# Kernel tuning notes

Hardware: AMD Instinct MI355X
Metric: run time of the kernel (lower is better)

## Reference

```python
import jax, jax.numpy as jnp
import numpy as np

EMBED = 1024
HEADS = 16
NQ = 32        # n_qubits_transformer
NQF = 32       # n_qubits_ffn
DK = NQ // HEADS
EPS = 1e-5


def layernorm(x, g, b):
    mu = jnp.mean(x, axis=-1, keepdims=True)
    var = jnp.var(x, axis=-1, keepdims=True)
    return (x - mu) * jax.lax.rsqrt(var + EPS) * g + b


def setup_inputs() -> dict:
    key = jax.random.key(0)
    ks = jax.random.split(key, 6)
    B, S = 8, 1024
    return {
        "x": jax.random.normal(ks[0], (B, S, EMBED), dtype=jnp.float32),
        "theta_attn": jax.random.normal(ks[1], (NQ,), dtype=jnp.float32),
        "theta_ffn": jax.random.normal(ks[2], (NQF,), dtype=jnp.float32),
        "w_combine": jax.random.normal(ks[3], (EMBED, NQ), dtype=jnp.float32) * 0.05,
        "w_ffn1": jax.random.normal(ks[4], (4096, NQF), dtype=jnp.float32) * 0.05,
        "w_ffn2": jax.random.normal(ks[5], (EMBED, 4096), dtype=jnp.float32) * 0.02,
        "g1": jnp.ones((EMBED,), jnp.float32),
        "b1": jnp.zeros((EMBED,), jnp.float32),
        "g2": jnp.ones((EMBED,), jnp.float32),
        "b2": jnp.zeros((EMBED,), jnp.float32),
    }


def quantum_measure(x_slice, theta):
    # |0> -RX(x)-> -RY(theta)-> <Z>  ==  cos(theta) * cos(x)  per wire (no entanglement)
    return jnp.cos(theta) * jnp.cos(x_slice)


def reference(x, theta_attn, theta_ffn, w_combine, w_ffn1, w_ffn2, g1, b1, g2, b2):
    B, S, _ = x.shape
    # --- quantum multi-head attention (q = k = v from circuit measurements) ---
    qv = quantum_measure(x[..., :NQ], theta_attn)                    # [B,S,NQ]
    q = qv.reshape(B, S, HEADS, DK).transpose(0, 2, 1, 3)            # [B,H,S,dk]
    scores = jnp.einsum("bhsd,bhtd->bhst", q, q) / jnp.sqrt(jnp.float32(DK))
    probs = jax.nn.softmax(scores, axis=-1)
    attn = jnp.einsum("bhst,bhtd->bhsd", probs, q)                   # [B,H,S,dk]
    attn = attn.transpose(0, 2, 1, 3).reshape(B, S, NQ)
    attn = attn @ w_combine.T                                        # [B,S,E]
    x1 = layernorm(x + attn, g1, b1)
    # --- quantum feed-forward ---
    qf = quantum_measure(x1[..., :NQF], theta_ffn)                   # [B,S,NQF]
    h = jax.nn.relu(qf @ w_ffn1.T)                                   # [B,S,ffn]
    ffn = h @ w_ffn2.T                                               # [B,S,E]
    return layernorm(x1 + ffn, g2, b2)
```

## Files before the change

kernel.cpp:

```cpp
#include <hip/hip_runtime.h>
#include <math.h>

#define EMB   1024
#define S_LEN 1024
#define NQ    32
#define HEADS 16
#define FFN   4096
#define T_TOK 8192
#define EPS   1e-5f
#define MiB   (1024ull * 1024ull)

typedef unsigned short u16;
typedef __attribute__((ext_vector_type(8))) short short8;
typedef __attribute__((ext_vector_type(4))) float float4_t;

__device__ __forceinline__ u16 f2bf(float f) {
    unsigned u = __float_as_uint(f);
    u += 0x7FFF + ((u >> 16) & 1);
    return (u16)(u >> 16);
}
__device__ __forceinline__ void async16(u16* lds, const u16* g) {
    __builtin_amdgcn_global_load_lds(
        (const __attribute__((address_space(1))) unsigned int*)g,
        (__attribute__((address_space(3))) unsigned int*)lds, 16, 0, 0);
}

#define N_W1 (FFN * NQ)
#define N_W2 (EMB * FFN)
#define N_WC (EMB * NQ)
__global__ __launch_bounds__(256) void k_prep(
        const float* __restrict__ w1, const float* __restrict__ w2,
        const float* __restrict__ wc, const float* __restrict__ x,
        const float* __restrict__ tha,
        u16* __restrict__ w1b, u16* __restrict__ w2b, u16* __restrict__ wcb,
        float* __restrict__ qv) {
    int idx = blockIdx.x * 256 + threadIdx.x;
    if (idx < T_TOK * NQ) {
        int i = idx & 31;
        int t = idx >> 5;
        int b = t >> 10, s = t & 1023;
        float cv = __cosf(tha[i]) * __cosf(x[(size_t)t * EMB + i]);
        int h = i >> 1, c = i & 1;
        qv[(((size_t)(b * HEADS + h)) * S_LEN + s) * 2 + c] = cv;
    }
    if (idx < N_W1)               w1b[idx] = f2bf(w1[idx]);
    else if (idx < N_W1 + N_W2)   w2b[idx - N_W1] = f2bf(w2[idx - N_W1]);
    else if (idx < N_W1 + N_W2 + N_WC) wcb[idx - N_W1 - N_W2] = f2bf(wc[idx - N_W1 - N_W2]);
}

__global__ __launch_bounds__(256) void k_attn(const float* __restrict__ qv,
                                              u16* __restrict__ attnB) {
    __shared__ __align__(16) float2 kv[S_LEN];
    int bh  = blockIdx.x;
    int tid = threadIdx.x;
    const float2* base = (const float2*)(qv + (size_t)bh * S_LEN * 2);
    for (int i = tid; i < S_LEN; i += 256) kv[i] = base[i];
    __syncthreads();
    int s = blockIdx.y * 256 + tid;
    float2 q = kv[s];
    float qx = q.x * 0.70710678f, qy = q.y * 0.70710678f;
    float den = 0.f, nx = 0.f, ny = 0.f;
#pragma unroll 4
    for (int t = 0; t < S_LEN; ++t) {
        float2 k = kv[t];
        float d = fmaf(qy, k.y, qx * k.x);
        float e = __expf(d);
        den += e;
        nx = fmaf(e, k.x, nx);
        ny = fmaf(e, k.y, ny);
    }
    float inv = 1.f / den;
    int b = bh >> 4, h = bh & 15;
    u16* o = attnB + (size_t)(b * S_LEN + s) * NQ + 2 * h;
    o[0] = f2bf(nx * inv);
    o[1] = f2bf(ny * inv);
}

__global__ __launch_bounds__(256) void k_combine_ln(
        const u16* __restrict__ A,
        const u16* __restrict__ B,
        const float* __restrict__ X,
        const float* __restrict__ g1, const float* __restrict__ b1,
        const float* __restrict__ thf,
        float* __restrict__ x1,
        u16* __restrict__ qf) {
    __shared__ float red[4][16][2];
    int tid = threadIdx.x, lane = tid & 63, wave = tid >> 6;
    int t0 = blockIdx.x * 16;
    int colbase = wave * 256;
    int rrow = (lane >> 4) * 4;
    short8 afr = *(const short8*)(A + (size_t)(t0 + (lane & 15)) * 32 + (lane >> 4) * 8);
    float4_t acc[16];
    float4_t zero = {0.f, 0.f, 0.f, 0.f};
#pragma unroll
    for (int tn = 0; tn < 16; ++tn) {
        short8 bfr = *(const short8*)(B + (size_t)(colbase + tn * 16 + (lane & 15)) * 32 + (lane >> 4) * 8);
        acc[tn] = __builtin_amdgcn_mfma_f32_16x16x32_bf16(afr, bfr, zero, 0, 0, 0);
    }
    float sm[4] = {0.f, 0.f, 0.f, 0.f}, sq[4] = {0.f, 0.f, 0.f, 0.f};
#pragma unroll
    for (int tn = 0; tn < 16; ++tn) {
        int nc = colbase + tn * 16 + (lane & 15);
#pragma unroll
        for (int r = 0; r < 4; ++r) {
            float v = acc[tn][r] + X[(size_t)(t0 + rrow + r) * EMB + nc];
            acc[tn][r] = v;
            sm[r] += v;
            sq[r] = fmaf(v, v, sq[r]);
        }
    }
#pragma unroll
    for (int o = 1; o < 16; o <<= 1) {
#pragma unroll
        for (int r = 0; r < 4; ++r) {
            sm[r] += __shfl_xor(sm[r], o, 64);
            sq[r] += __shfl_xor(sq[r], o, 64);
        }
    }
    if ((lane & 15) == 0) {
#pragma unroll
        for (int r = 0; r < 4; ++r) {
            red[wave][rrow + r][0] = sm[r];
            red[wave][rrow + r][1] = sq[r];
        }
    }
    __syncthreads();
    float mu[4], rs[4];
#pragma unroll
    for (int r = 0; r < 4; ++r) {
        float s = red[0][rrow + r][0] + red[1][rrow + r][0] +
                  red[2][rrow + r][0] + red[3][rrow + r][0];
        float q = red[0][rrow + r][1] + red[1][rrow + r][1] +
                  red[2][rrow + r][1] + red[3][rrow + r][1];
        float m = s * (1.f / EMB);
        mu[r] = m;
        rs[r] = rsqrtf(q * (1.f / EMB) - m * m + EPS);
    }
#pragma unroll
    for (int tn = 0; tn < 16; ++tn) {
        int nc = colbase + tn * 16 + (lane & 15);
        float g = g1[nc], bb = b1[nc];
#pragma unroll
        for (int r = 0; r < 4; ++r) {
            float y = (acc[tn][r] - mu[r]) * rs[r] * g + bb;
            x1[(size_t)(t0 + rrow + r) * EMB + nc] = y;
            if (nc < NQ)
                qf[(size_t)(t0 + rrow + r) * NQ + nc] = f2bf(__cosf(thf[nc]) * __cosf(y));
        }
    }
}

__global__ __launch_bounds__(256) void k_h(
        const u16* __restrict__ QF,
        const u16* __restrict__ W1,
        u16* __restrict__ H) {
    __shared__ __align__(16) u16 sA[128 * 32];
    __shared__ __align__(16) u16 sB[128 * 32];
    int tid = threadIdx.x, lane = tid & 63, wave = tid >> 6;
    int m0 = blockIdx.y * 128, n0 = blockIdx.x * 128;
    int wm = (wave >> 1) * 64, wn = (wave & 1) * 64;
    int srow = lane >> 2, scol = (lane & 3) * 8;
#pragma unroll
    for (int i = 0; i < 2; ++i) {
        int rb = wave * 32 + i * 16;
        async16(&sA[(size_t)rb * 32], QF + (size_t)(m0 + rb + srow) * 32 + scol);
        async16(&sB[(size_t)rb * 32], W1 + (size_t)(n0 + rb + srow) * 32 + scol);
    }
    __syncthreads();
    short8 af[4], bfr[4];
#pragma unroll
    for (int tm = 0; tm < 4; ++tm)
        af[tm] = *(const short8*)&sA[(size_t)(wm + tm * 16 + (lane & 15)) * 32 + (lane >> 4) * 8];
#pragma unroll
    for (int tn = 0; tn < 4; ++tn)
        bfr[tn] = *(const short8*)&sB[(size_t)(wn + tn * 16 + (lane & 15)) * 32 + (lane >> 4) * 8];
    float4_t zero = {0.f, 0.f, 0.f, 0.f};
#pragma unroll
    for (int tm = 0; tm < 4; ++tm) {
        int mr = m0 + wm + tm * 16 + (lane >> 4) * 4;
#pragma unroll
        for (int tn = 0; tn < 4; ++tn) {
            float4_t acc = __builtin_amdgcn_mfma_f32_16x16x32_bf16(af[tm], bfr[tn], zero, 0, 0, 0);
            int nc = n0 + wn + tn * 16 + (lane & 15);
#pragma unroll
            for (int r = 0; r < 4; ++r)
                H[(size_t)(mr + r) * FFN + nc] = f2bf(fmaxf(acc[r], 0.f));
        }
    }
}

__global__ __launch_bounds__(256, 2) void k_ffn2_db(
        const u16* __restrict__ H,
        const u16* __restrict__ W2,
        const float* __restrict__ X1,
        float* __restrict__ Y) {
    __shared__ __align__(16) u16 smem[32768];
    const int tid = threadIdx.x, lane = tid & 63, wave = tid >> 6;
    const int wm = wave >> 1, wn = wave & 1;

    int bid = blockIdx.x;
    int lid = (bid & 7) * 64 + (bid >> 3);
    const int m0 = (lid >> 3) * 128, n0 = (lid & 7) * 128;

    u16* A0 = smem;          u16* B0 = smem + 8192;
    u16* A1 = smem + 16384;  u16* B1 = smem + 24576;

    const int srow = tid >> 3;
    const int scol = ((tid & 7) ^ (srow & 7)) << 3;
    const int cb0 = ((0  + ((lane >> 4) * 16)) ^ ((lane & 7) << 4)) >> 1;
    const int cb1 = ((64 + ((lane >> 4) * 16)) ^ ((lane & 7) << 4)) >> 1;
    const int arow = lane & 15;

    auto stage = [&](u16* sA, u16* sB, int kt) {
#pragma unroll
        for (int j = 0; j < 4; ++j)
            async16(sA + (j * 32 + wave * 8) * 64,
                    H + (size_t)(m0 + j * 32 + srow) * FFN + kt + scol);
#pragma unroll
        for (int j = 0; j < 4; ++j)
            async16(sB + (j * 32 + wave * 8) * 64,
                    W2 + (size_t)(n0 + j * 32 + srow) * FFN + kt + scol);
    };

    float4_t acc[4][4];
    float4_t zero = {0.f, 0.f, 0.f, 0.f};
#pragma unroll
    for (int i = 0; i < 4; ++i)
#pragma unroll
        for (int j = 0; j < 4; ++j) acc[i][j] = zero;

    u16 *cA = A0, *cB = B0, *nA = A1, *nB = B1;
    stage(cA, cB, 0);

#pragma unroll 1
    for (int t = 0; t < 64; ++t) {
        if (t + 1 < 64) {
            stage(nA, nB, (t + 1) * 64);
            asm volatile("s_waitcnt vmcnt(8)" ::: "memory");
        } else {
            asm volatile("s_waitcnt vmcnt(0)" ::: "memory");
        }
        __builtin_amdgcn_s_barrier();

        short8 af0[4], af1[4], bf0[4], bf1[4];
#pragma unroll
        for (int f = 0; f < 4; ++f) {
            af0[f] = *(const short8*)(cA + (wm * 64 + f * 16 + arow) * 64 + cb0);
            af1[f] = *(const short8*)(cA + (wm * 64 + f * 16 + arow) * 64 + cb1);
        }
#pragma unroll
        for (int f = 0; f < 4; ++f) {
            bf0[f] = *(const short8*)(cB + (wn * 64 + f * 16 + arow) * 64 + cb0);
            bf1[f] = *(const short8*)(cB + (wn * 64 + f * 16 + arow) * 64 + cb1);
        }
        __builtin_amdgcn_s_setprio(1);
#pragma unroll
        for (int i = 0; i < 4; ++i)
#pragma unroll
            for (int j = 0; j < 4; ++j)
                acc[i][j] = __builtin_amdgcn_mfma_f32_16x16x32_bf16(af0[i], bf0[j], acc[i][j], 0, 0, 0);
#pragma unroll
        for (int i = 0; i < 4; ++i)
#pragma unroll
            for (int j = 0; j < 4; ++j)
                acc[i][j] = __builtin_amdgcn_mfma_f32_16x16x32_bf16(af1[i], bf1[j], acc[i][j], 0, 0, 0);
        __builtin_amdgcn_s_setprio(0);
        __builtin_amdgcn_s_barrier();

        u16* tA = cA; cA = nA; nA = tA;
        u16* tB = cB; cB = nB; nB = tB;
    }

#pragma unroll
    for (int i = 0; i < 4; ++i) {
        int mr = m0 + wm * 64 + i * 16 + (lane >> 4) * 4;
#pragma unroll
        for (int j = 0; j < 4; ++j) {
            int nc = n0 + wn * 64 + j * 16 + (lane & 15);
#pragma unroll
            for (int r = 0; r < 4; ++r) {
                size_t off = (size_t)(mr + r) * EMB + nc;
                Y[off] = acc[i][j][r] + X1[off];
            }
        }
    }
}

__global__ __launch_bounds__(256) void k_ffn_fused(
        const u16* __restrict__ QF,
        const u16* __restrict__ W1,
        const u16* __restrict__ W2,
        const float* __restrict__ X1,
        float* __restrict__ Y) {
    const int K = FFN, N = EMB;
    __shared__ __align__(16) u16 sW[64 * 32];
    __shared__ __align__(16) u16 sA[128 * 64];
    __shared__ __align__(16) u16 sB[128 * 64];
    int tid = threadIdx.x, lane = tid & 63, wave = tid >> 6;
    int m0 = blockIdx.y * 128, n0 = blockIdx.x * 128;
    int wm = (wave >> 1) * 64, wn = (wave & 1) * 64;

    short8 aq[2];
#pragma unroll
    for (int tm2 = 0; tm2 < 2; ++tm2) {
        int m = m0 + wave * 32 + tm2 * 16 + (lane & 15);
        aq[tm2] = *(const short8*)(QF + (size_t)m * 32 + (lane >> 4) * 8);
    }
    const u16* gB = W2 + (size_t)(n0 + wave * 32 + (lane >> 3)) * K + (lane & 7) * 8;
    const u16* gW = W1 + (size_t)(wave * 16 + (lane >> 2)) * 32 + (lane & 3) * 8;

    float4_t acc[4][4];
    float4_t zero = {0.f, 0.f, 0.f, 0.f};
#pragma unroll
    for (int tm = 0; tm < 4; ++tm)
#pragma unroll
        for (int tn = 0; tn < 4; ++tn) acc[tm][tn] = zero;

    for (int kt = 0; kt < K; kt += 64) {
        async16(&sW[(size_t)(wave * 16) * 32], gW + (size_t)kt * 32);
#pragma unroll
        for (int i = 0; i < 4; ++i)
            async16(&sB[(size_t)(wave * 32 + i * 8) * 64], gB + (size_t)i * 8 * K + kt);
        __syncthreads();

        int r0 = (lane >> 4) * 4;
#pragma unroll
        for (int tm2 = 0; tm2 < 2; ++tm2) {
            int mrow = wave * 32 + tm2 * 16;
#pragma unroll
            for (int tf = 0; tf < 4; ++tf) {
                short8 bw = *(const short8*)&sW[(size_t)(tf * 16 + (lane & 15)) * 32 + (lane >> 4) * 8];
                float4_t d = __builtin_amdgcn_mfma_f32_16x16x32_bf16(aq[tm2], bw, zero, 0, 0, 0);
                int cc = tf * 16 + (lane & 15);
#pragma unroll
                for (int r = 0; r < 4; ++r)
                    sA[(size_t)(mrow + r0 + r) * 64 + cc] = f2bf(fmaxf(d[r], 0.f));
            }
        }
        __syncthreads();

#pragma unroll
        for (int kk = 0; kk < 2; ++kk) {
            short8 af[4], bfr[4];
#pragma unroll
            for (int tm = 0; tm < 4; ++tm)
                af[tm] = *(const short8*)&sA[(size_t)(wm + tm * 16 + (lane & 15)) * 64 + kk * 32 + (lane >> 4) * 8];
#pragma unroll
            for (int tn = 0; tn < 4; ++tn)
                bfr[tn] = *(const short8*)&sB[(size_t)(wn + tn * 16 + (lane & 15)) * 64 + kk * 32 + (lane >> 4) * 8];
#pragma unroll
            for (int tm = 0; tm < 4; ++tm)
#pragma unroll
                for (int tn = 0; tn < 4; ++tn)
                    acc[tm][tn] = __builtin_amdgcn_mfma_f32_16x16x32_bf16(af[tm], bfr[tn], acc[tm][tn], 0, 0, 0);
        }
        __syncthreads();
    }
#pragma unroll
    for (int tm = 0; tm < 4; ++tm) {
        int mr = m0 + wm + tm * 16 + (lane >> 4) * 4;
#pragma unroll
        for (int tn = 0; tn < 4; ++tn) {
            int nc = n0 + wn + tn * 16 + (lane & 15);
#pragma unroll
            for (int r = 0; r < 4; ++r) {
                size_t off = (size_t)(mr + r) * N + nc;
                Y[off] = acc[tm][tn][r] + X1[off];
            }
        }
    }
}

__global__ __launch_bounds__(256) void k_ln2(float* __restrict__ y,
                                             const float* __restrict__ g2,
                                             const float* __restrict__ b2) {
    __shared__ float red[8];
    int t = blockIdx.x;
    int tid = threadIdx.x, lane = tid & 63, wave = tid >> 6;
    int e0 = tid * 4;
    float* row = y + (size_t)t * EMB;
    float4 v4 = *(const float4*)(row + e0);
    float v[4] = {v4.x, v4.y, v4.z, v4.w};
    float sm = v[0] + v[1] + v[2] + v[3];
    float sq = v[0]*v[0] + v[1]*v[1] + v[2]*v[2] + v[3]*v[3];
    for (int o = 32; o > 0; o >>= 1) {
        sm += __shfl_xor(sm, o, 64);
        sq += __shfl_xor(sq, o, 64);
    }
    if (lane == 0) { red[wave * 2] = sm; red[wave * 2 + 1] = sq; }
    __syncthreads();
    sm = red[0] + red[2] + red[4] + red[6];
    sq = red[1] + red[3] + red[5] + red[7];
    float mu  = sm * (1.f / EMB);
    float var = sq * (1.f / EMB) - mu * mu;
    float rs  = rsqrtf(var + EPS);
    float4 o4;
    o4.x = (v[0] - mu) * rs * g2[e0 + 0] + b2[e0 + 0];
    o4.y = (v[1] - mu) * rs * g2[e0 + 1] + b2[e0 + 1];
    o4.z = (v[2] - mu) * rs * g2[e0 + 2] + b2[e0 + 2];
    o4.w = (v[3] - mu) * rs * g2[e0 + 3] + b2[e0 + 3];
    *(float4*)(row + e0) = o4;
}

extern "C" void kernel_launch(void* const* d_in, const int* in_sizes, int n_in,
                              void* d_out, int out_size, void* d_ws, size_t ws_size,
                              hipStream_t stream) {
    const float* x   = (const float*)d_in[0];
    const float* tha = (const float*)d_in[1];
    const float* thf = (const float*)d_in[2];
    const float* wc  = (const float*)d_in[3];
    const float* w1  = (const float*)d_in[4];
    const float* w2  = (const float*)d_in[5];
    const float* g1  = (const float*)d_in[6];
    const float* b1  = (const float*)d_in[7];
    const float* g2  = (const float*)d_in[8];
    const float* b2  = (const float*)d_in[9];
    float* out = (float*)d_out;

    char* ws = (char*)d_ws;
    float* x1    = (float*)(ws);
    float* qv    = (float*)(ws + 32 * MiB);
    u16*   attnB = (u16*)  (ws + 33 * MiB);
    u16*   qf    = (u16*)  (ws + 34 * MiB);
    u16*   w1b   = (u16*)  (ws + 35 * MiB);
    u16*   w2b   = (u16*)  (ws + 36 * MiB);
    u16*   wcb   = (u16*)  (ws + 44 * MiB);
    u16*   hbuf  = (u16*)  (ws + 48 * MiB);

    const bool split = ws_size >= (size_t)112 * MiB;

    k_prep<<<(N_W1 + N_W2 + N_WC + 255) / 256, 256, 0, stream>>>(
        w1, w2, wc, x, tha, w1b, w2b, wcb, qv);
    k_attn<<<dim3(128, 4), 256, 0, stream>>>(qv, attnB);
    k_combine_ln<<<T_TOK / 16, 256, 0, stream>>>(
        attnB, wcb, x, g1, b1, thf, x1, qf);
    if (split) {
        k_h<<<dim3(FFN / 128, T_TOK / 128), 256, 0, stream>>>(qf, w1b, hbuf);
        k_ffn2_db<<<dim3(512), 256, 0, stream>>>(hbuf, w2b, x1, out);
    } else {
        k_ffn_fused<<<dim3(EMB / 128, T_TOK / 128), 256, 0, stream>>>(
            qf, w1b, w2b, x1, out);
    }
    k_ln2<<<T_TOK, 256, 0, stream>>>(out, g2, b2);
}
```

Before: 251.3 us.

## Fuse all stages into one cooperative persistent kernel with grid syncs

Replaces the sequence of six kernel launches with a single cooperative kernel of 512 blocks that runs each stage (prep, attention, combine+LN, FFN1, FFN2, LN2) separated by grid-wide syncs. The aim is to remove launch overhead and inter-kernel gaps. In exchange, stages that previously used more blocks (prep, k_h, LN2) now loop over work with a fixed grid, grid.sync adds its own cost, and occupancy is capped by the largest stage's shared memory and registers. The old multi-kernel path is kept as a fallback if the cooperative launch fails.

```diff
diff --git a/kernel.cpp b/kernel.cpp
--- a/kernel.cpp
+++ b/kernel.cpp
@@ -1,5 +1,8 @@
 #include <hip/hip_runtime.h>
+#include <hip/hip_cooperative_groups.h>
 #include <math.h>
+
+namespace cg = cooperative_groups;
 
 #define EMB   1024
 #define S_LEN 1024
@@ -28,6 +31,298 @@
 #define N_W1 (FFN * NQ)
 #define N_W2 (EMB * FFN)
 #define N_WC (EMB * NQ)
+#define NPREP ((N_W1 + N_W2 + N_WC) / 256)
+
+__global__ __launch_bounds__(256, 2) void k_mega(
+        const float* __restrict__ w1, const float* __restrict__ w2,
+        const float* __restrict__ wc, const float* __restrict__ x,
+        const float* __restrict__ tha, const float* __restrict__ thf,
+        const float* __restrict__ g1, const float* __restrict__ b1,
+        const float* __restrict__ g2, const float* __restrict__ b2,
+        u16* __restrict__ w1b, u16* __restrict__ w2b, u16* __restrict__ wcb,
+        float* __restrict__ qv, u16* __restrict__ attnB, u16* __restrict__ qf,
+        float* __restrict__ x1, u16* __restrict__ hbuf,
+        float* __restrict__ out) {
+    __shared__ __align__(16) u16 smem[32768];
+    cg::grid_group grid = cg::this_grid();
+    const int bid = blockIdx.x;
+    const int tid = threadIdx.x, lane = tid & 63, wave = tid >> 6;
+
+    for (int vb = bid; vb < NPREP; vb += 512) {
+        int idx = vb * 256 + tid;
+        if (idx < T_TOK * NQ) {
+            int i = idx & 31;
+            int t = idx >> 5;
+            int b = t >> 10, s = t & 1023;
+            float cv = __cosf(tha[i]) * __cosf(x[(size_t)t * EMB + i]);
+            int h = i >> 1, c = i & 1;
+            qv[(((size_t)(b * HEADS + h)) * S_LEN + s) * 2 + c] = cv;
+        }
+        if (idx < N_W1)               w1b[idx] = f2bf(w1[idx]);
+        else if (idx < N_W1 + N_W2)   w2b[idx - N_W1] = f2bf(w2[idx - N_W1]);
+        else if (idx < N_W1 + N_W2 + N_WC) wcb[idx - N_W1 - N_W2] = f2bf(wc[idx - N_W1 - N_W2]);
+    }
+    __threadfence();
+    grid.sync();
+
+    {
+        float2* kv = (float2*)smem;
+        int bh = bid >> 2;
+        const float2* base = (const float2*)(qv + (size_t)bh * S_LEN * 2);
+        for (int i = tid; i < S_LEN; i += 256) kv[i] = base[i];
+        __syncthreads();
+        int s = (bid & 3) * 256 + tid;
+        float2 q = kv[s];
+        float qx = q.x * 0.70710678f, qy = q.y * 0.70710678f;
+        float den = 0.f, nx = 0.f, ny = 0.f;
+#pragma unroll 4
+        for (int t = 0; t < S_LEN; ++t) {
+            float2 k = kv[t];
+            float d = fmaf(qy, k.y, qx * k.x);
+            float e = __expf(d);
+            den += e;
+            nx = fmaf(e, k.x, nx);
+            ny = fmaf(e, k.y, ny);
+        }
+        float inv = 1.f / den;
+        int b = bh >> 4, h = bh & 15;
+        u16* o = attnB + (size_t)(b * S_LEN + s) * NQ + 2 * h;
+        o[0] = f2bf(nx * inv);
+        o[1] = f2bf(ny * inv);
+    }
+    __threadfence();
+    grid.sync();
+
+    {
+        float (*red)[16][2] = (float (*)[16][2])smem;
+        int t0 = bid * 16;
+        int colbase = wave * 256;
+        int rrow = (lane >> 4) * 4;
+        short8 afr = *(const short8*)(attnB + (size_t)(t0 + (lane & 15)) * 32 + (lane >> 4) * 8);
+        float4_t acc[16];
+        float4_t zero = {0.f, 0.f, 0.f, 0.f};
+#pragma unroll
+        for (int tn = 0; tn < 16; ++tn) {
+            short8 bfr = *(const short8*)(wcb + (size_t)(colbase + tn * 16 + (lane & 15)) * 32 + (lane >> 4) * 8);
+            acc[tn] = __builtin_amdgcn_mfma_f32_16x16x32_bf16(afr, bfr, zero, 0, 0, 0);
+        }
+        float sm[4] = {0.f, 0.f, 0.f, 0.f}, sq[4] = {0.f, 0.f, 0.f, 0.f};
+#pragma unroll
+        for (int tn = 0; tn < 16; ++tn) {
+            int nc = colbase + tn * 16 + (lane & 15);
+#pragma unroll
+            for (int r = 0; r < 4; ++r) {
+                float v = acc[tn][r] + x[(size_t)(t0 + rrow + r) * EMB + nc];
+                acc[tn][r] = v;
+                sm[r] += v;
+                sq[r] = fmaf(v, v, sq[r]);
+            }
+        }
+#pragma unroll
+        for (int o = 1; o < 16; o <<= 1) {
+#pragma unroll
+            for (int r = 0; r < 4; ++r) {
+                sm[r] += __shfl_xor(sm[r], o, 64);
+                sq[r] += __shfl_xor(sq[r], o, 64);
+            }
+        }
+        if ((lane & 15) == 0) {
+#pragma unroll
+            for (int r = 0; r < 4; ++r) {
+                red[wave][rrow + r][0] = sm[r];
+                red[wave][rrow + r][1] = sq[r];
+            }
+        }
+        __syncthreads();
+        float mu[4], rs[4];
+#pragma unroll
+        for (int r = 0; r < 4; ++r) {
+            float s = red[0][rrow + r][0] + red[1][rrow + r][0] +
+                      red[2][rrow + r][0] + red[3][rrow + r][0];
+            float q = red[0][rrow + r][1] + red[1][rrow + r][1] +
+                      red[2][rrow + r][1] + red[3][rrow + r][1];
+            float m = s * (1.f / EMB);
+            mu[r] = m;
+            rs[r] = rsqrtf(q * (1.f / EMB) - m * m + EPS);
+        }
+#pragma unroll
+        for (int tn = 0; tn < 16; ++tn) {
+            int nc = colbase + tn * 16 + (lane & 15);
+            float g = g1[nc], bb = b1[nc];
+#pragma unroll
+            for (int r = 0; r < 4; ++r) {
+                float y = (acc[tn][r] - mu[r]) * rs[r] * g + bb;
+                x1[(size_t)(t0 + rrow + r) * EMB + nc] = y;
+                if (nc < NQ)
+                    qf[(size_t)(t0 + rrow + r) * NQ + nc] = f2bf(__cosf(thf[nc]) * __cosf(y));
+            }
+        }
+    }
+    __threadfence();
+    grid.sync();
+
+    {
+        u16* sA = smem;
+        u16* sB = smem + 4096;
+        int wm = (wave >> 1) * 64, wn = (wave & 1) * 64;
+        int srow = lane >> 2, scol = (lane & 3) * 8;
+        for (int v = bid; v < 2048; v += 512) {
+            int n0 = (v & 31) * 128, m0 = (v >> 5) * 128;
+#pragma unroll
+            for (int i = 0; i < 2; ++i) {
+                int rb = wave * 32 + i * 16;
+                async16(sA + (size_t)rb * 32, qf  + (size_t)(m0 + rb + srow) * 32 + scol);
+                async16(sB + (size_t)rb * 32, w1b + (size_t)(n0 + rb + srow) * 32 + scol);
+            }
+            __syncthreads();
+            short8 af[4], bfr[4];
+#pragma unroll
+            for (int tm = 0; tm < 4; ++tm)
+                af[tm] = *(const short8*)(sA + (size_t)(wm + tm * 16 + (lane & 15)) * 32 + (lane >> 4) * 8);
+#pragma unroll
+            for (int tn = 0; tn < 4; ++tn)
+                bfr[tn] = *(const short8*)(sB + (size_t)(wn + tn * 16 + (lane & 15)) * 32 + (lane >> 4) * 8);
+            float4_t zero = {0.f, 0.f, 0.f, 0.f};
+#pragma unroll
+            for (int tm = 0; tm < 4; ++tm) {
+                int mr = m0 + wm + tm * 16 + (lane >> 4) * 4;
+#pragma unroll
+                for (int tn = 0; tn < 4; ++tn) {
+                    float4_t acc = __builtin_amdgcn_mfma_f32_16x16x32_bf16(af[tm], bfr[tn], zero, 0, 0, 0);
+                    int nc = n0 + wn + tn * 16 + (lane & 15);
+#pragma unroll
+                    for (int r = 0; r < 4; ++r)
+                        hbuf[(size_t)(mr + r) * FFN + nc] = f2bf(fmaxf(acc[r], 0.f));
+                }
+            }
+            __syncthreads();
+        }
+    }
+    __threadfence();
+    grid.sync();
+
+    {
+        const int wm = wave >> 1, wn = wave & 1;
+        int lid = (bid & 7) * 64 + (bid >> 3);
+        const int m0 = (lid >> 3) * 128, n0 = (lid & 7) * 128;
+
+        u16* A0 = smem;          u16* B0 = smem + 8192;
+        u16* A1 = smem + 16384;  u16* B1 = smem + 24576;
+
+        const int srow = tid >> 3;
+        const int scol = ((tid & 7) ^ (srow & 7)) << 3;
+        const int cb0 = ((0  + ((lane >> 4) * 16)) ^ ((lane & 7) << 4)) >> 1;
+        const int cb1 = ((64 + ((lane >> 4) * 16)) ^ ((lane & 7) << 4)) >> 1;
+        const int arow = lane & 15;
+
+        auto stage = [&](u16* sA, u16* sB, int kt) {
+#pragma unroll
+            for (int j = 0; j < 4; ++j)
+                async16(sA + (j * 32 + wave * 8) * 64,
+                        hbuf + (size_t)(m0 + j * 32 + srow) * FFN + kt + scol);
+#pragma unroll
+            for (int j = 0; j < 4; ++j)
+                async16(sB + (j * 32 + wave * 8) * 64,
+                        w2b + (size_t)(n0 + j * 32 + srow) * FFN + kt + scol);
+        };
+
+        float4_t acc[4][4];
+        float4_t zero = {0.f, 0.f, 0.f, 0.f};
+#pragma unroll
+        for (int i = 0; i < 4; ++i)
+#pragma unroll
+            for (int j = 0; j < 4; ++j) acc[i][j] = zero;
+
+        u16 *cA = A0, *cB = B0, *nA = A1, *nB = B1;
+        stage(cA, cB, 0);
+
+#pragma unroll 1
+        for (int t = 0; t < 64; ++t) {
+            if (t + 1 < 64) {
+                stage(nA, nB, (t + 1) * 64);
+                asm volatile("s_waitcnt vmcnt(8)" ::: "memory");
+            } else {
+                asm volatile("s_waitcnt vmcnt(0)" ::: "memory");
+            }
+            __builtin_amdgcn_s_barrier();
+
+            short8 af0[4], af1[4], bf0[4], bf1[4];
+#pragma unroll
+            for (int f = 0; f < 4; ++f) {
+                af0[f] = *(const short8*)(cA + (wm * 64 + f * 16 + arow) * 64 + cb0);
+                af1[f] = *(const short8*)(cA + (wm * 64 + f * 16 + arow) * 64 + cb1);
+            }
+#pragma unroll
+            for (int f = 0; f < 4; ++f) {
+                bf0[f] = *(const short8*)(cB + (wn * 64 + f * 16 + arow) * 64 + cb0);
+                bf1[f] = *(const short8*)(cB + (wn * 64 + f * 16 + arow) * 64 + cb1);
+            }
+            __builtin_amdgcn_s_setprio(1);
+#pragma unroll
+            for (int i = 0; i < 4; ++i)
+#pragma unroll
+                for (int j = 0; j < 4; ++j)
+                    acc[i][j] = __builtin_amdgcn_mfma_f32_16x16x32_bf16(af0[i], bf0[j], acc[i][j], 0, 0, 0);
+#pragma unroll
+            for (int i = 0; i < 4; ++i)
+#pragma unroll
+                for (int j = 0; j < 4; ++j)
+                    acc[i][j] = __builtin_amdgcn_mfma_f32_16x16x32_bf16(af1[i], bf1[j], acc[i][j], 0, 0, 0);
+            __builtin_amdgcn_s_setprio(0);
+            __builtin_amdgcn_s_barrier();
+
+            u16* tA = cA; cA = nA; nA = tA;
+            u16* tB = cB; cB = nB; nB = tB;
+        }
+
+#pragma unroll
+        for (int i = 0; i < 4; ++i) {
+            int mr = m0 + wm * 64 + i * 16 + (lane >> 4) * 4;
+#pragma unroll
+            for (int j = 0; j < 4; ++j) {
+                int nc = n0 + wn * 64 + j * 16 + (lane & 15);
+#pragma unroll
+                for (int r = 0; r < 4; ++r) {
+                    size_t off = (size_t)(mr + r) * EMB + nc;
+                    out[off] = acc[i][j][r] + x1[off];
+                }
+            }
+        }
+    }
+    __threadfence();
+    grid.sync();
+
+    {
+        float* red = (float*)smem;
+        for (int t = bid; t < T_TOK; t += 512) {
+            int e0 = tid * 4;
+            float* row = out + (size_t)t * EMB;
+            float4 v4 = *(const float4*)(row + e0);
+            float v[4] = {v4.x, v4.y, v4.z, v4.w};
+            float sm = v[0] + v[1] + v[2] + v[3];
+            float sq = v[0]*v[0] + v[1]*v[1] + v[2]*v[2] + v[3]*v[3];
+            for (int o = 32; o > 0; o >>= 1) {
+                sm += __shfl_xor(sm, o, 64);
+                sq += __shfl_xor(sq, o, 64);
+            }
+            if (lane == 0) { red[wave * 2] = sm; red[wave * 2 + 1] = sq; }
+            __syncthreads();
+            sm = red[0] + red[2] + red[4] + red[6];
+            sq = red[1] + red[3] + red[5] + red[7];
+            float mu  = sm * (1.f / EMB);
+            float var = sq * (1.f / EMB) - mu * mu;
+            float rs  = rsqrtf(var + EPS);
+            float4 o4;
+            o4.x = (v[0] - mu) * rs * g2[e0 + 0] + b2[e0 + 0];
+            o4.y = (v[1] - mu) * rs * g2[e0 + 1] + b2[e0 + 1];
+            o4.z = (v[2] - mu) * rs * g2[e0 + 2] + b2[e0 + 2];
+            o4.w = (v[3] - mu) * rs * g2[e0 + 3] + b2[e0 + 3];
+            *(float4*)(row + e0) = o4;
+            __syncthreads();
+        }
+    }
+}
+
 __global__ __launch_bounds__(256) void k_prep(
         const float* __restrict__ w1, const float* __restrict__ w2,
         const float* __restrict__ wc, const float* __restrict__ x,
@@ -77,13 +372,11 @@
 }
 
 __global__ __launch_bounds__(256) void k_combine_ln(
-        const u16* __restrict__ A,
-        const u16* __restrict__ B,
+        const u16* __restrict__ A, const u16* __restrict__ B,
         const float* __restrict__ X,
         const float* __restrict__ g1, const float* __restrict__ b1,
         const float* __restrict__ thf,
-        float* __restrict__ x1,
-        u16* __restrict__ qf) {
+        float* __restrict__ x1, u16* __restrict__ qf) {
     __shared__ float red[4][16][2];
     int tid = threadIdx.x, lane = tid & 63, wave = tid >> 6;
     int t0 = blockIdx.x * 16;
@@ -151,8 +444,7 @@
 }
 
 __global__ __launch_bounds__(256) void k_h(
-        const u16* __restrict__ QF,
-        const u16* __restrict__ W1,
+        const u16* __restrict__ QF, const u16* __restrict__ W1,
         u16* __restrict__ H) {
     __shared__ __align__(16) u16 sA[128 * 32];
     __shared__ __align__(16) u16 sB[128 * 32];
@@ -190,27 +482,21 @@
 }
 
 __global__ __launch_bounds__(256, 2) void k_ffn2_db(
-        const u16* __restrict__ H,
-        const u16* __restrict__ W2,
-        const float* __restrict__ X1,
-        float* __restrict__ Y) {
+        const u16* __restrict__ H, const u16* __restrict__ W2,
+        const float* __restrict__ X1, float* __restrict__ Y) {
     __shared__ __align__(16) u16 smem[32768];
     const int tid = threadIdx.x, lane = tid & 63, wave = tid >> 6;
     const int wm = wave >> 1, wn = wave & 1;
-
     int bid = blockIdx.x;
     int lid = (bid & 7) * 64 + (bid >> 3);
     const int m0 = (lid >> 3) * 128, n0 = (lid & 7) * 128;
-
     u16* A0 = smem;          u16* B0 = smem + 8192;
     u16* A1 = smem + 16384;  u16* B1 = smem + 24576;
-
     const int srow = tid >> 3;
     const int scol = ((tid & 7) ^ (srow & 7)) << 3;
     const int cb0 = ((0  + ((lane >> 4) * 16)) ^ ((lane & 7) << 4)) >> 1;
     const int cb1 = ((64 + ((lane >> 4) * 16)) ^ ((lane & 7) << 4)) >> 1;
     const int arow = lane & 15;
-
     auto stage = [&](u16* sA, u16* sB, int kt) {
 #pragma unroll
         for (int j = 0; j < 4; ++j)
@@ -221,17 +507,14 @@
             async16(sB + (j * 32 + wave * 8) * 64,
                     W2 + (size_t)(n0 + j * 32 + srow) * FFN + kt + scol);
     };
-
     float4_t acc[4][4];
     float4_t zero = {0.f, 0.f, 0.f, 0.f};
 #pragma unroll
     for (int i = 0; i < 4; ++i)
 #pragma unroll
         for (int j = 0; j < 4; ++j) acc[i][j] = zero;
-
     u16 *cA = A0, *cB = B0, *nA = A1, *nB = B1;
     stage(cA, cB, 0);
-
 #pragma unroll 1
     for (int t = 0; t < 64; ++t) {
         if (t + 1 < 64) {
@@ -241,7 +524,6 @@
             asm volatile("s_waitcnt vmcnt(0)" ::: "memory");
         }
         __builtin_amdgcn_s_barrier();
-
         short8 af0[4], af1[4], bf0[4], bf1[4];
 #pragma unroll
         for (int f = 0; f < 4; ++f) {
@@ -266,11 +548,9 @@
                 acc[i][j] = __builtin_amdgcn_mfma_f32_16x16x32_bf16(af1[i], bf1[j], acc[i][j], 0, 0, 0);
         __builtin_amdgcn_s_setprio(0);
         __builtin_amdgcn_s_barrier();
-
         u16* tA = cA; cA = nA; nA = tA;
         u16* tB = cB; cB = nB; nB = tB;
     }
-
 #pragma unroll
     for (int i = 0; i < 4; ++i) {
         int mr = m0 + wm * 64 + i * 16 + (lane >> 4) * 4;
@@ -287,10 +567,8 @@
 }
 
 __global__ __launch_bounds__(256) void k_ffn_fused(
-        const u16* __restrict__ QF,
-        const u16* __restrict__ W1,
-        const u16* __restrict__ W2,
-        const float* __restrict__ X1,
+        const u16* __restrict__ QF, const u16* __restrict__ W1,
+        const u16* __restrict__ W2, const float* __restrict__ X1,
         float* __restrict__ Y) {
     const int K = FFN, N = EMB;
     __shared__ __align__(16) u16 sW[64 * 32];
@@ -299,7 +577,6 @@
     int tid = threadIdx.x, lane = tid & 63, wave = tid >> 6;
     int m0 = blockIdx.y * 128, n0 = blockIdx.x * 128;
     int wm = (wave >> 1) * 64, wn = (wave & 1) * 64;
-
     short8 aq[2];
 #pragma unroll
     for (int tm2 = 0; tm2 < 2; ++tm2) {
@@ -308,21 +585,18 @@
     }
     const u16* gB = W2 + (size_t)(n0 + wave * 32 + (lane >> 3)) * K + (lane & 7) * 8;
     const u16* gW = W1 + (size_t)(wave * 16 + (lane >> 2)) * 32 + (lane & 3) * 8;
-
     float4_t acc[4][4];
     float4_t zero = {0.f, 0.f, 0.f, 0.f};
 #pragma unroll
     for (int tm = 0; tm < 4; ++tm)
 #pragma unroll
         for (int tn = 0; tn < 4; ++tn) acc[tm][tn] = zero;
-
     for (int kt = 0; kt < K; kt += 64) {
         async16(&sW[(size_t)(wave * 16) * 32], gW + (size_t)kt * 32);
 #pragma unroll
         for (int i = 0; i < 4; ++i)
             async16(&sB[(size_t)(wave * 32 + i * 8) * 64], gB + (size_t)i * 8 * K + kt);
         __syncthreads();
-
         int r0 = (lane >> 4) * 4;
 #pragma unroll
         for (int tm2 = 0; tm2 < 2; ++tm2) {
@@ -338,7 +612,6 @@
             }
         }
         __syncthreads();
-
 #pragma unroll
         for (int kk = 0; kk < 2; ++kk) {
             short8 af[4], bfr[4];
@@ -429,8 +702,20 @@
 
     const bool split = ws_size >= (size_t)112 * MiB;
 
-    k_prep<<<(N_W1 + N_W2 + N_WC + 255) / 256, 256, 0, stream>>>(
-        w1, w2, wc, x, tha, w1b, w2b, wcb, qv);
+    if (split) {
+        void* args[] = {
+            (void*)&w1, (void*)&w2, (void*)&wc, (void*)&x,
+            (void*)&tha, (void*)&thf, (void*)&g1, (void*)&b1,
+            (void*)&g2, (void*)&b2,
+            (void*)&w1b, (void*)&w2b, (void*)&wcb,
+            (void*)&qv, (void*)&attnB, (void*)&qf,
+            (void*)&x1, (void*)&hbuf, (void*)&out};
+        hipError_t e = hipLaunchCooperativeKernel(
+            (const void*)k_mega, dim3(512), dim3(256), args, 0, stream);
+        if (e == hipSuccess) return;
+    }
+
+    k_prep<<<NPREP, 256, 0, stream>>>(w1, w2, wc, x, tha, w1b, w2b, wcb, qv);
     k_attn<<<dim3(128, 4), 256, 0, stream>>>(qv, attnB);
     k_combine_ln<<<T_TOK / 16, 256, 0, stream>>>(
         attnB, wcb, x, g1, b1, thf, x1, qf);
```

Result: slower. 814.6 us (+224.1%).

## Fuse quantum measure into attention and FFN1 into combine-layernorm kernel

Applied to the files above, without the earlier changes.

Folds the attention-side cosine measurement into the attention kernel, which now reads x directly and no longer goes through a qv buffer. Weight bf16 conversion moves into extra blocks of the same launch. In the split path, the FFN1 GEMM plus ReLU is computed inside the combine+layernorm kernel from a shared-memory qf tile, which drops the separate k_h launch and the qf round trip. This cuts two launches and intermediate traffic, but the fused kernel now reads W1 from global memory with uncoalesced per-block loads and writes H with scattered stores.

```diff
diff --git a/kernel.cpp b/kernel.cpp
--- a/kernel.cpp
+++ b/kernel.cpp
@@ -28,35 +28,36 @@
 #define N_W1 (FFN * NQ)
 #define N_W2 (EMB * FFN)
 #define N_WC (EMB * NQ)
-__global__ __launch_bounds__(256) void k_prep(
+#define NWBLK ((N_W1 + N_W2 + N_WC) / 256)
+
+__global__ __launch_bounds__(256) void k_attn_prep(
+        const float* __restrict__ x,  const float* __restrict__ tha,
         const float* __restrict__ w1, const float* __restrict__ w2,
-        const float* __restrict__ wc, const float* __restrict__ x,
-        const float* __restrict__ tha,
+        const float* __restrict__ wc,
         u16* __restrict__ w1b, u16* __restrict__ w2b, u16* __restrict__ wcb,
-        float* __restrict__ qv) {
-    int idx = blockIdx.x * 256 + threadIdx.x;
-    if (idx < T_TOK * NQ) {
-        int i = idx & 31;
-        int t = idx >> 5;
-        int b = t >> 10, s = t & 1023;
-        float cv = __cosf(tha[i]) * __cosf(x[(size_t)t * EMB + i]);
-        int h = i >> 1, c = i & 1;
-        qv[(((size_t)(b * HEADS + h)) * S_LEN + s) * 2 + c] = cv;
-    }
-    if (idx < N_W1)               w1b[idx] = f2bf(w1[idx]);
-    else if (idx < N_W1 + N_W2)   w2b[idx - N_W1] = f2bf(w2[idx - N_W1]);
-    else if (idx < N_W1 + N_W2 + N_WC) wcb[idx - N_W1 - N_W2] = f2bf(wc[idx - N_W1 - N_W2]);
-}
-
-__global__ __launch_bounds__(256) void k_attn(const float* __restrict__ qv,
-                                              u16* __restrict__ attnB) {
+        u16* __restrict__ attnB) {
     __shared__ __align__(16) float2 kv[S_LEN];
-    int bh  = blockIdx.x;
+    int bid = blockIdx.x;
     int tid = threadIdx.x;
-    const float2* base = (const float2*)(qv + (size_t)bh * S_LEN * 2);
-    for (int i = tid; i < S_LEN; i += 256) kv[i] = base[i];
+
+    if (bid >= 512) {
+        int idx = (bid - 512) * 256 + tid;
+        if (idx < N_W1)               w1b[idx] = f2bf(w1[idx]);
+        else if (idx < N_W1 + N_W2)   w2b[idx - N_W1] = f2bf(w2[idx - N_W1]);
+        else if (idx < N_W1 + N_W2 + N_WC) wcb[idx - N_W1 - N_W2] = f2bf(wc[idx - N_W1 - N_W2]);
+        return;
+    }
+
+    int bh = bid >> 2;
+    int b = bh >> 4, h = bh & 15;
+    float c0 = __cosf(tha[2 * h]);
+    float c1 = __cosf(tha[2 * h + 1]);
+    for (int i = tid; i < S_LEN; i += 256) {
+        float2 xv = *(const float2*)(x + (size_t)(b * S_LEN + i) * EMB + 2 * h);
+        kv[i] = make_float2(c0 * __cosf(xv.x), c1 * __cosf(xv.y));
+    }
     __syncthreads();
-    int s = blockIdx.y * 256 + tid;
+    int s = (bid & 3) * 256 + tid;
     float2 q = kv[s];
     float qx = q.x * 0.70710678f, qy = q.y * 0.70710678f;
     float den = 0.f, nx = 0.f, ny = 0.f;
@@ -70,20 +71,191 @@
         ny = fmaf(e, k.y, ny);
     }
     float inv = 1.f / den;
-    int b = bh >> 4, h = bh & 15;
     u16* o = attnB + (size_t)(b * S_LEN + s) * NQ + 2 * h;
     o[0] = f2bf(nx * inv);
     o[1] = f2bf(ny * inv);
 }
 
-__global__ __launch_bounds__(256) void k_combine_ln(
+__global__ __launch_bounds__(256) void k_combine_ln_h(
         const u16* __restrict__ A,
         const u16* __restrict__ B,
         const float* __restrict__ X,
         const float* __restrict__ g1, const float* __restrict__ b1,
         const float* __restrict__ thf,
+        const u16* __restrict__ W1,
         float* __restrict__ x1,
-        u16* __restrict__ qf) {
+        u16* __restrict__ H) {
+    __shared__ float red[4][16][2];
+    __shared__ __align__(16) u16 qfl[16 * 32];
+    int tid = threadIdx.x, lane = tid & 63, wave = tid >> 6;
+    int t0 = blockIdx.x * 16;
+    int colbase = wave * 256;
+    int rrow = (lane >> 4) * 4;
+    short8 afr = *(const short8*)(A + (size_t)(t0 + (lane & 15)) * 32 + (lane >> 4) * 8);
+    float4_t acc[16];
+    float4_t zero = {0.f, 0.f, 0.f, 0.f};
+#pragma unroll
+    for (int tn = 0; tn < 16; ++tn) {
+        short8 bfr = *(const short8*)(B + (size_t)(colbase + tn * 16 + (lane & 15)) * 32 + (lane >> 4) * 8);
+        acc[tn] = __builtin_amdgcn_mfma_f32_16x16x32_bf16(afr, bfr, zero, 0, 0, 0);
+    }
+    float sm[4] = {0.f, 0.f, 0.f, 0.f}, sq[4] = {0.f, 0.f, 0.f, 0.f};
+#pragma unroll
+    for (int tn = 0; tn < 16; ++tn) {
+        int nc = colbase + tn * 16 + (lane & 15);
+#pragma unroll
+        for (int r = 0; r < 4; ++r) {
+            float v = acc[tn][r] + X[(size_t)(t0 + rrow + r) * EMB + nc];
+            acc[tn][r] = v;
+            sm[r] += v;
+            sq[r] = fmaf(v, v, sq[r]);
+        }
+    }
+#pragma unroll
+    for (int o = 1; o < 16; o <<= 1) {
+#pragma unroll
+        for (int r = 0; r < 4; ++r) {
+            sm[r] += __shfl_xor(sm[r], o, 64);
+            sq[r] += __shfl_xor(sq[r], o, 64);
+        }
+    }
+    if ((lane & 15) == 0) {
+#pragma unroll
+        for (int r = 0; r < 4; ++r) {
+            red[wave][rrow + r][0] = sm[r];
+            red[wave][rrow + r][1] = sq[r];
+        }
+    }
+    __syncthreads();
+    float mu[4], rs[4];
+#pragma unroll
+    for (int r = 0; r < 4; ++r) {
+        float s = red[0][rrow + r][0] + red[1][rrow + r][0] +
+                  red[2][rrow + r][0] + red[3][rrow + r][0];
+        float q = red[0][rrow + r][1] + red[1][rrow + r][1] +
+                  red[2][rrow + r][1] + red[3][rrow + r][1];
+        float m = s * (1.f / EMB);
+        mu[r] = m;
+        rs[r] = rsqrtf(q * (1.f / EMB) - m * m + EPS);
+    }
+#pragma unroll
+    for (int tn = 0; tn < 16; ++tn) {
+        int nc = colbase + tn * 16 + (lane & 15);
+        float g = g1[nc], bb = b1[nc];
+#pragma unroll
+        for (int r = 0; r < 4; ++r) {
+            float y = (acc[tn][r] - mu[r]) * rs[r] * g + bb;
+            x1[(size_t)(t0 + rrow + r) * EMB + nc] = y;
+            if (nc < NQ)
+                qfl[(rrow + r) * 32 + nc] = f2bf(__cosf(thf[nc]) * __cosf(y));
+        }
+    }
+    __syncthreads();
+
+    short8 afr2 = *(const short8*)&qfl[(lane & 15) * 32 + (lane >> 4) * 8];
+#pragma unroll 4
+    for (int tn2 = 0; tn2 < 64; ++tn2) {
+        int ncol = wave * 1024 + tn2 * 16;
+        short8 bfr = *(const short8*)(W1 + (size_t)(ncol + (lane & 15)) * 32 + (lane >> 4) * 8);
+        float4_t d = __builtin_amdgcn_mfma_f32_16x16x32_bf16(afr2, bfr, zero, 0, 0, 0);
+        int cc = ncol + (lane & 15);
+#pragma unroll
+        for (int r = 0; r < 4; ++r)
+            H[(size_t)(t0 + rrow + r) * FFN + cc] = f2bf(fmaxf(d[r], 0.f));
+    }
+}
+
+__global__ __launch_bounds__(256, 2) void k_ffn2_db(
+        const u16* __restrict__ H, const u16* __restrict__ W2,
+        const float* __restrict__ X1, float* __restrict__ Y) {
+    __shared__ __align__(16) u16 smem[32768];
+    const int tid = threadIdx.x, lane = tid & 63, wave = tid >> 6;
+    const int wm = wave >> 1, wn = wave & 1;
+    int bid = blockIdx.x;
+    int lid = (bid & 7) * 64 + (bid >> 3);
+    const int m0 = (lid >> 3) * 128, n0 = (lid & 7) * 128;
+    u16* A0 = smem;          u16* B0 = smem + 8192;
+    u16* A1 = smem + 16384;  u16* B1 = smem + 24576;
+    const int srow = tid >> 3;
+    const int scol = ((tid & 7) ^ (srow & 7)) << 3;
+    const int cb0 = ((0  + ((lane >> 4) * 16)) ^ ((lane & 7) << 4)) >> 1;
+    const int cb1 = ((64 + ((lane >> 4) * 16)) ^ ((lane & 7) << 4)) >> 1;
+    const int arow = lane & 15;
+    auto stage = [&](u16* sA, u16* sB, int kt) {
+#pragma unroll
+        for (int j = 0; j < 4; ++j)
+            async16(sA + (j * 32 + wave * 8) * 64,
+                    H + (size_t)(m0 + j * 32 + srow) * FFN + kt + scol);
+#pragma unroll
+        for (int j = 0; j < 4; ++j)
+            async16(sB + (j * 32 + wave * 8) * 64,
+                    W2 + (size_t)(n0 + j * 32 + srow) * FFN + kt + scol);
+    };
+    float4_t acc[4][4];
+    float4_t zero = {0.f, 0.f, 0.f, 0.f};
+#pragma unroll
+    for (int i = 0; i < 4; ++i)
+#pragma unroll
+        for (int j = 0; j < 4; ++j) acc[i][j] = zero;
+    u16 *cA = A0, *cB = B0, *nA = A1, *nB = B1;
+    stage(cA, cB, 0);
+#pragma unroll 1
+    for (int t = 0; t < 64; ++t) {
+        if (t + 1 < 64) {
+            stage(nA, nB, (t + 1) * 64);
+            asm volatile("s_waitcnt vmcnt(8)" ::: "memory");
+        } else {
+            asm volatile("s_waitcnt vmcnt(0)" ::: "memory");
+        }
+        __builtin_amdgcn_s_barrier();
+        short8 af0[4], af1[4], bf0[4], bf1[4];
+#pragma unroll
+        for (int f = 0; f < 4; ++f) {
+            af0[f] = *(const short8*)(cA + (wm * 64 + f * 16 + arow) * 64 + cb0);
+            af1[f] = *(const short8*)(cA + (wm * 64 + f * 16 + arow) * 64 + cb1);
+        }
+#pragma unroll
+        for (int f = 0; f < 4; ++f) {
+            bf0[f] = *(const short8*)(cB + (wn * 64 + f * 16 + arow) * 64 + cb0);
+            bf1[f] = *(const short8*)(cB + (wn * 64 + f * 16 + arow) * 64 + cb1);
+        }
+        __builtin_amdgcn_s_setprio(1);
+#pragma unroll
+        for (int i = 0; i < 4; ++i)
+#pragma unroll
+            for (int j = 0; j < 4; ++j)
+                acc[i][j] = __builtin_amdgcn_mfma_f32_16x16x32_bf16(af0[i], bf0[j], acc[i][j], 0, 0, 0);
+#pragma unroll
+        for (int i = 0; i < 4; ++i)
+#pragma unroll
+            for (int j = 0; j < 4; ++j)
+                acc[i][j] = __builtin_amdgcn_mfma_f32_16x16x32_bf16(af1[i], bf1[j], acc[i][j], 0, 0, 0);
+        __builtin_amdgcn_s_setprio(0);
+        __builtin_amdgcn_s_barrier();
+        u16* tA = cA; cA = nA; nA = tA;
+        u16* tB = cB; cB = nB; nB = tB;
+    }
+#pragma unroll
+    for (int i = 0; i < 4; ++i) {
+        int mr = m0 + wm * 64 + i * 16 + (lane >> 4) * 4;
+#pragma unroll
+        for (int j = 0; j < 4; ++j) {
+            int nc = n0 + wn * 64 + j * 16 + (lane & 15);
+#pragma unroll
+            for (int r = 0; r < 4; ++r) {
+                size_t off = (size_t)(mr + r) * EMB + nc;
+                Y[off] = acc[i][j][r] + X1[off];
+            }
+        }
+    }
+}
+
+__global__ __launch_bounds__(256) void k_combine_ln(
+        const u16* __restrict__ A, const u16* __restrict__ B,
+        const float* __restrict__ X,
+        const float* __restrict__ g1, const float* __restrict__ b1,
+        const float* __restrict__ thf,
+        float* __restrict__ x1, u16* __restrict__ qf) {
     __shared__ float red[4][16][2];
     int tid = threadIdx.x, lane = tid & 63, wave = tid >> 6;
     int t0 = blockIdx.x * 16;
@@ -150,147 +322,9 @@
     }
 }
 
-__global__ __launch_bounds__(256) void k_h(
-        const u16* __restrict__ QF,
-        const u16* __restrict__ W1,
-        u16* __restrict__ H) {
-    __shared__ __align__(16) u16 sA[128 * 32];
-    __shared__ __align__(16) u16 sB[128 * 32];
-    int tid = threadIdx.x, lane = tid & 63, wave = tid >> 6;
-    int m0 = blockIdx.y * 128, n0 = blockIdx.x * 128;
-    int wm = (wave >> 1) * 64, wn = (wave & 1) * 64;
-    int srow = lane >> 2, scol = (lane & 3) * 8;
-#pragma unroll
-    for (int i = 0; i < 2; ++i) {
-        int rb = wave * 32 + i * 16;
-        async16(&sA[(size_t)rb * 32], QF + (size_t)(m0 + rb + srow) * 32 + scol);
-        async16(&sB[(size_t)rb * 32], W1 + (size_t)(n0 + rb + srow) * 32 + scol);
-    }
-    __syncthreads();
-    short8 af[4], bfr[4];
-#pragma unroll
-    for (int tm = 0; tm < 4; ++tm)
-        af[tm] = *(const short8*)&sA[(size_t)(wm + tm * 16 + (lane & 15)) * 32 + (lane >> 4) * 8];
-#pragma unroll
-    for (int tn = 0; tn < 4; ++tn)
-        bfr[tn] = *(const short8*)&sB[(size_t)(wn + tn * 16 + (lane & 15)) * 32 + (lane >> 4) * 8];
-    float4_t zero = {0.f, 0.f, 0.f, 0.f};
-#pragma unroll
-    for (int tm = 0; tm < 4; ++tm) {
-        int mr = m0 + wm + tm * 16 + (lane >> 4) * 4;
-#pragma unroll
-        for (int tn = 0; tn < 4; ++tn) {
-            float4_t acc = __builtin_amdgcn_mfma_f32_16x16x32_bf16(af[tm], bfr[tn], zero, 0, 0, 0);
-            int nc = n0 + wn + tn * 16 + (lane & 15);
-#pragma unroll
-            for (int r = 0; r < 4; ++r)
-                H[(size_t)(mr + r) * FFN + nc] = f2bf(fmaxf(acc[r], 0.f));
-        }
-    }
-}
-
-__global__ __launch_bounds__(256, 2) void k_ffn2_db(
-        const u16* __restrict__ H,
-        const u16* __restrict__ W2,
-        const float* __restrict__ X1,
-        float* __restrict__ Y) {
-    __shared__ __align__(16) u16 smem[32768];
-    const int tid = threadIdx.x, lane = tid & 63, wave = tid >> 6;
-    const int wm = wave >> 1, wn = wave & 1;
-
-    int bid = blockIdx.x;
-    int lid = (bid & 7) * 64 + (bid >> 3);
-    const int m0 = (lid >> 3) * 128, n0 = (lid & 7) * 128;
-
-    u16* A0 = smem;          u16* B0 = smem + 8192;
-    u16* A1 = smem + 16384;  u16* B1 = smem + 24576;
-
-    const int srow = tid >> 3;
-    const int scol = ((tid & 7) ^ (srow & 7)) << 3;
-    const int cb0 = ((0  + ((lane >> 4) * 16)) ^ ((lane & 7) << 4)) >> 1;
-    const int cb1 = ((64 + ((lane >> 4) * 16)) ^ ((lane & 7) << 4)) >> 1;
-    const int arow = lane & 15;
-
-    auto stage = [&](u16* sA, u16* sB, int kt) {
-#pragma unroll
-        for (int j = 0; j < 4; ++j)
-            async16(sA + (j * 32 + wave * 8) * 64,
-                    H + (size_t)(m0 + j * 32 + srow) * FFN + kt + scol);
-#pragma unroll
-        for (int j = 0; j < 4; ++j)
-            async16(sB + (j * 32 + wave * 8) * 64,
-                    W2 + (size_t)(n0 + j * 32 + srow) * FFN + kt + scol);
-    };
-
-    float4_t acc[4][4];
-    float4_t zero = {0.f, 0.f, 0.f, 0.f};
-#pragma unroll
-    for (int i = 0; i < 4; ++i)
-#pragma unroll
-        for (int j = 0; j < 4; ++j) acc[i][j] = zero;
-
-    u16 *cA = A0, *cB = B0, *nA = A1, *nB = B1;
-    stage(cA, cB, 0);
-
-#pragma unroll 1
-    for (int t = 0; t < 64; ++t) {
-        if (t + 1 < 64) {
-            stage(nA, nB, (t + 1) * 64);
-            asm volatile("s_waitcnt vmcnt(8)" ::: "memory");
-        } else {
-            asm volatile("s_waitcnt vmcnt(0)" ::: "memory");
-        }
-        __builtin_amdgcn_s_barrier();
-
-        short8 af0[4], af1[4], bf0[4], bf1[4];
-#pragma unroll
-        for (int f = 0; f < 4; ++f) {
-            af0[f] = *(const short8*)(cA + (wm * 64 + f * 16 + arow) * 64 + cb0);
-            af1[f] = *(const short8*)(cA + (wm * 64 + f * 16 + arow) * 64 + cb1);
-        }
-#pragma unroll
-        for (int f = 0; f < 4; ++f) {
-            bf0[f] = *(const short8*)(cB + (wn * 64 + f * 16 + arow) * 64 + cb0);
-            bf1[f] = *(const short8*)(cB + (wn * 64 + f * 16 + arow) * 64 + cb1);
-        }
-        __builtin_amdgcn_s_setprio(1);
-#pragma unroll
-        for (int i = 0; i < 4; ++i)
-#pragma unroll
-            for (int j = 0; j < 4; ++j)
-                acc[i][j] = __builtin_amdgcn_mfma_f32_16x16x32_bf16(af0[i], bf0[j], acc[i][j], 0, 0, 0);
-#pragma unroll
-        for (int i = 0; i < 4; ++i)
-#pragma unroll
-            for (int j = 0; j < 4; ++j)
-                acc[i][j] = __builtin_amdgcn_mfma_f32_16x16x32_bf16(af1[i], bf1[j], acc[i][j], 0, 0, 0);
-        __builtin_amdgcn_s_setprio(0);
-        __builtin_amdgcn_s_barrier();
-
-        u16* tA = cA; cA = nA; nA = tA;
-        u16* tB = cB; cB = nB; nB = tB;
-    }
-
-#pragma unroll
-    for (int i = 0; i < 4; ++i) {
-        int mr = m0 + wm * 64 + i * 16 + (lane >> 4) * 4;
-#pragma unroll
-        for (int j = 0; j < 4; ++j) {
-            int nc = n0 + wn * 64 + j * 16 + (lane & 15);
-#pragma unroll
-            for (int r = 0; r < 4; ++r) {
-                size_t off = (size_t)(mr + r) * EMB + nc;
-                Y[off] = acc[i][j][r] + X1[off];
-            }
-        }
-    }
-}
-
 __global__ __launch_bounds__(256) void k_ffn_fused(
-        const u16* __restrict__ QF,
-        const u16* __restrict__ W1,
-        const u16* __restrict__ W2,
-        const float* __restrict__ X1,
+        const u16* __restrict__ QF, const u16* __restrict__ W1,
+        const u16* __restrict__ W2, const float* __restrict__ X1,
         float* __restrict__ Y) {
     const int K = FFN, N = EMB;
     __shared__ __align__(16) u16 sW[64 * 32];
@@ -299,7 +333,6 @@
     int tid = threadIdx.x, lane = tid & 63, wave = tid >> 6;
     int m0 = blockIdx.y * 128, n0 = blockIdx.x * 128;
     int wm = (wave >> 1) * 64, wn = (wave & 1) * 64;
-
     short8 aq[2];
 #pragma unroll
     for (int tm2 = 0; tm2 < 2; ++tm2) {
@@ -308,21 +341,18 @@
     }
     const u16* gB = W2 + (size_t)(n0 + wave * 32 + (lane >> 3)) * K + (lane & 7) * 8;
     const u16* gW = W1 + (size_t)(wave * 16 + (lane >> 2)) * 32 + (lane & 3) * 8;
-
     float4_t acc[4][4];
     float4_t zero = {0.f, 0.f, 0.f, 0.f};
 #pragma unroll
     for (int tm = 0; tm < 4; ++tm)
 #pragma unroll
         for (int tn = 0; tn < 4; ++tn) acc[tm][tn] = zero;
-
     for (int kt = 0; kt < K; kt += 64) {
         async16(&sW[(size_t)(wave * 16) * 32], gW + (size_t)kt * 32);
 #pragma unroll
         for (int i = 0; i < 4; ++i)
             async16(&sB[(size_t)(wave * 32 + i * 8) * 64], gB + (size_t)i * 8 * K + kt);
         __syncthreads();
-
         int r0 = (lane >> 4) * 4;
 #pragma unroll
         for (int tm2 = 0; tm2 < 2; ++tm2) {
@@ -338,7 +368,6 @@
             }
         }
         __syncthreads();
-
 #pragma unroll
         for (int kk = 0; kk < 2; ++kk) {
             short8 af[4], bfr[4];
@@ -419,7 +448,6 @@
 
     char* ws = (char*)d_ws;
     float* x1    = (float*)(ws);
-    float* qv    = (float*)(ws + 32 * MiB);
     u16*   attnB = (u16*)  (ws + 33 * MiB);
     u16*   qf    = (u16*)  (ws + 34 * MiB);
     u16*   w1b   = (u16*)  (ws + 35 * MiB);
@@ -429,15 +457,15 @@
 
     const bool split = ws_size >= (size_t)112 * MiB;
 
-    k_prep<<<(N_W1 + N_W2 + N_WC + 255) / 256, 256, 0, stream>>>(
-        w1, w2, wc, x, tha, w1b, w2b, wcb, qv);
-    k_attn<<<dim3(128, 4), 256, 0, stream>>>(qv, attnB);
-    k_combine_ln<<<T_TOK / 16, 256, 0, stream>>>(
-        attnB, wcb, x, g1, b1, thf, x1, qf);
+    k_attn_prep<<<512 + NWBLK, 256, 0, stream>>>(
+        x, tha, w1, w2, wc, w1b, w2b, wcb, attnB);
     if (split) {
-        k_h<<<dim3(FFN / 128, T_TOK / 128), 256, 0, stream>>>(qf, w1b, hbuf);
+        k_combine_ln_h<<<T_TOK / 16, 256, 0, stream>>>(
+            attnB, wcb, x, g1, b1, thf, w1b, x1, hbuf);
         k_ffn2_db<<<dim3(512), 256, 0, stream>>>(hbuf, w2b, x1, out);
     } else {
+        k_combine_ln<<<T_TOK / 16, 256, 0, stream>>>(
+            attnB, wcb, x, g1, b1, thf, x1, qf);
         k_ffn_fused<<<dim3(EMB / 128, T_TOK / 128), 256, 0, stream>>>(
             qf, w1b, w2b, x1, out);
     }
```

New measurement: 250.5 us. Within noise of the previous version (-0.3%).
